# Optimization experiments

Hardware: AMD Instinct MI355X
Metric: run time of the kernel (lower is better)

The kernel has to match this reference:

```python
import jax, jax.numpy as jnp
import numpy as np

R = 8            # in_channels: number of relation graphs
C = 4            # out_channels
E = 2_000_000    # edges per relation graph


def setup_inputs() -> dict:
    key = jax.random.key(0)
    k1, k2 = jax.random.split(key)
    # Per-relation edge weights g.edata['w'] for each of the R relation graphs.
    edge_w = jax.random.uniform(k1, (R, E), dtype=jnp.float32)
    # Learned relation-mixing weight, init std=0.01 as in reset_parameters.
    weight = jax.random.normal(k2, (C, R), dtype=jnp.float32) * 0.01
    return {"edge_w": edge_w, "weight": weight}


def reference(edge_w, weight):
    # Filter = softmax over relations (dim=1), as softmax_flag=True.
    Filter = jax.nn.softmax(weight, axis=1)                    # [C, R]
    # adj_sum_graph(A, 'w_sum') sums the sparse adjacencies; in COO form
    # (with per-relation edge lists concatenated) the summed graph's edge
    # weights are just the scalar-scaled per-relation edge weights.
    # out[c, r, e] = Filter[c, r] * edge_w[r, e]
    out = Filter[:, :, None] * edge_w[None, :, :]              # [C, R, E]
    return out, Filter
```

## Files before the change

kernel.cpp:

```cpp
#include <hip/hip_runtime.h>

#define RREL 8
#define COUT 4
#define NEDGE 2000000
#define E4   (NEDGE / 4)
#define N4   (RREL * E4)

__global__ void gtconv_filter_kernel(const float* __restrict__ weight,
                                     float* __restrict__ filter_out) {
    int c = threadIdx.x;
    if (c < COUT) {
        float v[RREL];
        float m = -3.402823e38f;
        #pragma unroll
        for (int r = 0; r < RREL; ++r) {
            v[r] = weight[c * RREL + r];
            m = fmaxf(m, v[r]);
        }
        float s = 0.0f;
        #pragma unroll
        for (int r = 0; r < RREL; ++r) {
            v[r] = expf(v[r] - m);
            s += v[r];
        }
        float inv = 1.0f / s;
        #pragma unroll
        for (int r = 0; r < RREL; ++r) {
            filter_out[c * RREL + r] = v[r] * inv;
        }
    }
}

__global__ void __launch_bounds__(256)
gtconv_scale_kernel(const float4* __restrict__ ew4,
                    const float* __restrict__ filter,
                    float4* __restrict__ out4) {
    __shared__ float sf[COUT * RREL];
    if (threadIdx.x < COUT * RREL) sf[threadIdx.x] = filter[threadIdx.x];
    __syncthreads();

    int idx = blockIdx.x * blockDim.x + threadIdx.x;
    if (idx >= N4) return;

    int r = idx / E4;
    float4 w = ew4[idx];

    #pragma unroll
    for (int c = 0; c < COUT; ++c) {
        float f = sf[c * RREL + r];
        float4 o;
        o.x = w.x * f;
        o.y = w.y * f;
        o.z = w.z * f;
        o.w = w.w * f;
        out4[(size_t)c * N4 + idx] = o;
    }
}

extern "C" void kernel_launch(void* const* d_in, const int* in_sizes, int n_in,
                              void* d_out, int out_size, void* d_ws, size_t ws_size,
                              hipStream_t stream) {
    const float* edge_w = (const float*)d_in[0];
    const float* weight = (const float*)d_in[1];
    float* out = (float*)d_out;

    float* filter_slot = out + (size_t)COUT * RREL * NEDGE;

    gtconv_filter_kernel<<<1, 64, 0, stream>>>(weight, filter_slot);

    int blocks = (N4 + 255) / 256;
    gtconv_scale_kernel<<<blocks, 256, 0, stream>>>(
        (const float4*)edge_w, filter_slot, (float4*)out);
}
```

Baseline: 298.5 us.

## Fuse softmax filter into scale kernel and use nontemporal loads/stores

Merges the separate softmax filter kernel into the scaling kernel: each block recomputes the 4x8 softmax into shared memory, and block 0 writes the filter output. This removes one kernel launch and the dependency on a global filter buffer. Edge-weight loads and output stores now use nontemporal builtins to avoid cache pollution on a pure streaming workload. The bounds check is dropped because N4 divides evenly by the block size, and expf becomes the faster __expf.

```diff
diff --git a/kernel.cpp b/kernel.cpp
--- a/kernel.cpp
+++ b/kernel.cpp
@@ -5,55 +5,53 @@
 #define NEDGE 2000000
 #define E4   (NEDGE / 4)
 #define N4   (RREL * E4)
+#define BLOCK 256
+#define GRID  (N4 / BLOCK)
 
-__global__ void gtconv_filter_kernel(const float* __restrict__ weight,
-                                     float* __restrict__ filter_out) {
-    int c = threadIdx.x;
-    if (c < COUT) {
+typedef float vfloat4 __attribute__((ext_vector_type(4)));
+
+__global__ void __launch_bounds__(BLOCK)
+gtconv_fused_kernel(const vfloat4* __restrict__ ew4,
+                    const float* __restrict__ weight,
+                    vfloat4* __restrict__ out4,
+                    float* __restrict__ filter_out) {
+    __shared__ float sf[COUT * RREL];
+
+    int t = threadIdx.x;
+    if (t < COUT) {
         float v[RREL];
         float m = -3.402823e38f;
         #pragma unroll
         for (int r = 0; r < RREL; ++r) {
-            v[r] = weight[c * RREL + r];
+            v[r] = weight[t * RREL + r];
             m = fmaxf(m, v[r]);
         }
         float s = 0.0f;
         #pragma unroll
         for (int r = 0; r < RREL; ++r) {
-            v[r] = expf(v[r] - m);
+            v[r] = __expf(v[r] - m);
             s += v[r];
         }
         float inv = 1.0f / s;
         #pragma unroll
         for (int r = 0; r < RREL; ++r) {
-            filter_out[c * RREL + r] = v[r] * inv;
+            float f = v[r] * inv;
+            sf[t * RREL + r] = f;
+            if (blockIdx.x == 0) filter_out[t * RREL + r] = f;
         }
     }
-}
-
-__global__ void __launch_bounds__(256)
-gtconv_scale_kernel(const float4* __restrict__ ew4,
-                    const float* __restrict__ filter,
-                    float4* __restrict__ out4) {
-    __shared__ float sf[COUT * RREL];
-    if (threadIdx.x < COUT * RREL) sf[threadIdx.x] = filter[threadIdx.x];
     __syncthreads();
 
-    int idx = blockIdx.x * blockDim.x + threadIdx.x;
-    if (idx >= N4) return;
+    int idx = blockIdx.x * BLOCK + t;
+    int r = idx / E4;
 
-    int r = idx / E4;
-    float4 w = ew4[idx];
+    vfloat4 w = __builtin_nontemporal_load(&ew4[idx]);
 
     #pragma unroll
     for (int c = 0; c < COUT; ++c) {
         float f = sf[c * RREL + r];
-        float4 o;
-        o.x = w.x * f;
-        o.y = w.y * f;
-        o.z = w.z * f;
-        o.w = w.w * f;
-        out4[(size_t)c * N4 + idx] = o;
+        vfloat4 o = w * f;
+        __builtin_nontemporal_store(o, &out4[(size_t)c * N4 + idx]);
     }
 }
 
@@ -66,9 +64,6 @@
 
     float* filter_slot = out + (size_t)COUT * RREL * NEDGE;
 
-    gtconv_filter_kernel<<<1, 64, 0, stream>>>(weight, filter_slot);
-
-    int blocks = (N4 + 255) / 256;
-    gtconv_scale_kernel<<<blocks, 256, 0, stream>>>(
-        (const float4*)edge_w, filter_slot, (float4*)out);
+    gtconv_fused_kernel<<<GRID, BLOCK, 0, stream>>>(
+        (const vfloat4*)edge_w, weight, (vfloat4*)out, filter_slot);
 }
```

After: 293.5 us. About the same (-1.7%).
